# Kernel tuning notes

Hardware: AMD Instinct MI355X
Metric: run time of the kernel (lower is better)

## Reference

```python
import jax, jax.numpy as jnp
import numpy as np

K_WRITE = 4
NUM_SLOTS = 16
VOCAB = 50257
D = 512


def layer_norm(x, g, b, eps=1e-5):
    mu = jnp.mean(x, axis=-1, keepdims=True)
    var = jnp.mean((x - mu) ** 2, axis=-1, keepdims=True)
    return (x - mu) * jax.lax.rsqrt(var + eps) * g + b


def setup_inputs() -> dict:
    key = jax.random.key(0)
    ks = jax.random.split(key, 16)
    B, T = 32, 2048
    s = lambda *sh: 1.0 / np.sqrt(sh[0])
    seq = jax.random.randint(ks[0], (B, T), 0, VOCAB)
    embed = jax.random.normal(ks[1], (VOCAB, D), jnp.float32) * 0.02
    W1 = jax.random.normal(ks[2], (D, 2 * D), jnp.float32) * s(D)
    b1 = jnp.zeros((2 * D,), jnp.float32)
    W2 = jax.random.normal(ks[3], (2 * D, D), jnp.float32) * s(2 * D)
    b2 = jnp.zeros((D,), jnp.float32)
    ln_g = jnp.ones((D,), jnp.float32)
    ln_b = jnp.zeros((D,), jnp.float32)
    Wg = jax.random.normal(ks[4], (D, NUM_SLOTS), jnp.float32) * s(D)
    bg = jnp.zeros((NUM_SLOTS,), jnp.float32)
    Wr = jax.random.normal(ks[5], (D, D), jnp.float32) * s(D)
    br = jnp.zeros((D,), jnp.float32)
    Wo = jax.random.normal(ks[6], (D, VOCAB), jnp.float32) * s(D)
    bo = jnp.zeros((VOCAB,), jnp.float32)
    return dict(seq=seq, embed=embed, W1=W1, b1=b1, W2=W2, b2=b2, ln_g=ln_g,
                ln_b=ln_b, Wg=Wg, bg=bg, Wr=Wr, br=br, Wo=Wo, bo=bo)


def forward(seq, embed, W1, b1, W2, b2, ln_g, ln_b, Wg, bg, Wr, br, Wo, bo):
    # Encoder: embed -> FFN residual -> layernorm
    h = embed[seq]                                  # [B,T,D]
    ff = jax.nn.relu(h @ W1 + b1) @ W2 + b2
    hiddens = layer_norm(h + ff, ln_g, ln_b)        # [B,T,D]

    ctx_h = hiddens[:, :-1, :]                      # [B,T-1,D]
    B, Tm1, Dd = ctx_h.shape
    k_w = min(K_WRITE, Tm1)

    # write_to_memory: gate -> topk -> gather -> scatter into zero memory
    gate_scores = jnp.mean(ctx_h @ Wg + bg, axis=-1)          # [B,T-1]
    _, top_idx = jax.lax.top_k(gate_scores, k_w)              # [B,k_w]
    gathered = jnp.take_along_axis(ctx_h, top_idx[:, :, None], axis=1)  # [B,k_w,D]
    slot_idx = jnp.arange(k_w) % NUM_SLOTS                    # unique since k_w<=slots
    mem = jnp.zeros((B, NUM_SLOTS, Dd), ctx_h.dtype).at[:, slot_idx, :].set(gathered)

    # small attention read
    q = hiddens[:, -1, :] @ Wr + br                 # [B,D]
    scores = jnp.einsum('bsd,bd->bs', mem, q)       # [B,slots]
    attn = jax.nn.softmax(scores, axis=-1)
    ctx = jnp.einsum('bs,bsd->bd', attn, mem)       # [B,D]
    return ctx @ Wo + bo                            # [B,vocab]


def reference(seq, embed, W1, b1, W2, b2, ln_g, ln_b, Wg, bg, Wr, br, Wo, bo):
    return forward(seq, embed, W1, b1, W2, b2, ln_g, ln_b, Wg, bg, Wr, br, Wo, bo)
```

## Files before the change

### kernel.cpp

```cpp
#include <hip/hip_runtime.h>
#include <stdint.h>

typedef __attribute__((ext_vector_type(8))) short bf16x8;
typedef __attribute__((ext_vector_type(4))) float f32x4;
typedef __attribute__((ext_vector_type(16))) float f32x16;
typedef unsigned short ushortT;

#define DEV static __device__ __forceinline__

DEV unsigned short f2bf(float x) {
  union { float f; unsigned u; } v; v.f = x;
  unsigned r = v.u + 0x7fffu + ((v.u >> 16) & 1u);
  return (unsigned short)(r >> 16);
}
DEV float bf2f(unsigned short b) {
  union { unsigned u; float f; } v; v.u = ((unsigned)b) << 16; return v.f;
}
DEV void gll16(const void* g, void* l) {
  __builtin_amdgcn_global_load_lds((const __attribute__((address_space(1))) void*)g,
                                   (__attribute__((address_space(3))) void*)l, 16, 0, 0);
}

#define VMW(n) asm volatile("s_waitcnt vmcnt(" #n ")" ::: "memory")
#define RAWBAR() __builtin_amdgcn_s_barrier()
#define SCHED0() __builtin_amdgcn_sched_barrier(0)

__global__ void kPrep(const float* __restrict__ W1, const float* __restrict__ W2,
                      const float* __restrict__ Wg, const float* __restrict__ ln_g,
                      ushortT* __restrict__ W1t, ushortT* __restrict__ W2t,
                      float* __restrict__ gw, float* __restrict__ wgm) {
  const size_t t = (size_t)blockIdx.x * 256 + threadIdx.x;
  if (t < 524288) {
    int n = (int)(t & 1023), k = (int)(t >> 10);
    W1t[(size_t)n * 512 + k] = f2bf(W1[(size_t)k * 1024 + n]);
  } else if (t < 1048576) {
    size_t u = t - 524288;
    int n = (int)(u & 511), k = (int)(u >> 9);
    W2t[(size_t)n * 1024 + k] = f2bf(W2[(size_t)k * 512 + n]);
  } else if (t < 1048576 + 512) {
    int c = (int)(t - 1048576);
    float s = 0.f;
    for (int j = 0; j < 16; ++j) s += Wg[c * 16 + j];
    float m = s * (1.0f / 16.0f);
    wgm[c] = m;
    gw[c] = ln_g[c] * m;
  }
}

__global__ void kPrep2(const float* __restrict__ gw, const float* __restrict__ wgm,
                       const float* __restrict__ ln_b, const float* __restrict__ bg,
                       float* __restrict__ consts) {
  const int tid = threadIdx.x;
  float a = gw[tid];
  float c = ln_b[tid] * wgm[tid];
  #pragma unroll
  for (int s = 1; s < 64; s <<= 1) { a += __shfl_xor(a, s); c += __shfl_xor(c, s); }
  __shared__ float red[8][2];
  const int wv = tid >> 6, ln = tid & 63;
  if (ln == 0) { red[wv][0] = a; red[wv][1] = c; }
  __syncthreads();
  if (tid == 0) {
    float Cg = 0, Cb0 = 0;
    for (int k = 0; k < 8; ++k) { Cg += red[k][0]; Cb0 += red[k][1]; }
    float bgm = 0;
    for (int j = 0; j < 16; ++j) bgm += bg[j];
    bgm *= (1.0f / 16.0f);
    consts[0] = Cg; consts[1] = Cb0 + bgm; consts[2] = bgm;
  }
}

__global__ void kEmbed(const int* __restrict__ seq, const float* __restrict__ embed,
                       ushortT* __restrict__ h) {
  const size_t t = (size_t)blockIdx.x * 256 + threadIdx.x;
  const size_t row = t >> 6;
  const int seg = (int)(t & 63) * 8;
  const int tok = seq[row];
  const float4* src = (const float4*)(embed + (size_t)tok * 512 + seg);
  float4 x = src[0], y = src[1];
  uint4 u;
  u.x = (unsigned)f2bf(x.x) | ((unsigned)f2bf(x.y) << 16);
  u.y = (unsigned)f2bf(x.z) | ((unsigned)f2bf(x.w) << 16);
  u.z = (unsigned)f2bf(y.x) | ((unsigned)f2bf(y.y) << 16);
  u.w = (unsigned)f2bf(y.z) | ((unsigned)f2bf(y.w) << 16);
  *(uint4*)(h + row * 512 + seg) = u;
}

__global__ __launch_bounds__(512, 2) void kG1p(const ushortT* __restrict__ h,
                                               const ushortT* __restrict__ W1t,
                                               const float* __restrict__ b1,
                                               ushortT* __restrict__ Y) {
  __shared__ __align__(16) ushortT SH[32768];
  const int tid = threadIdx.x, w = tid >> 6, l = tid & 63;
  const int b = blockIdx.x, xcd = b & 7, loc = b >> 3;
  const int nt = loc & 3, mtl = loc >> 2;
  const size_t m0 = (size_t)(xcd * 16 + mtl) * 256;
  const int n0 = nt * 256;
  const int rl = l & 15, gq = l >> 4;
  f32x4 acc[4][8] = {};

  auto stage = [&](int buf, int k0) {
    #pragma unroll
    for (int q = 0; q < 2; ++q) {
      const int c = w * 2 + q;
      gll16(h + (m0 + c * 16 + rl) * 512 + k0 + gq * 8, &SH[buf * 8192 + c * 512]);
      gll16(W1t + (size_t)(n0 + c * 16 + rl) * 512 + k0 + gq * 8, &SH[16384 + buf * 8192 + c * 512]);
    }
  };

  const int wr = w >> 1, wc = w & 1, l8 = l * 8;
  auto compute = [&](int buf) {
    bf16x8 a[4], bb[8];
    #pragma unroll
    for (int i = 0; i < 4; ++i)
      a[i] = *(const bf16x8*)&SH[buf * 8192 + (wr * 4 + i) * 512 + l8];
    #pragma unroll
    for (int j = 0; j < 8; ++j)
      bb[j] = *(const bf16x8*)&SH[16384 + buf * 8192 + (wc * 8 + j) * 512 + l8];
    #pragma unroll
    for (int i = 0; i < 4; ++i)
      #pragma unroll
      for (int j = 0; j < 8; ++j)
        acc[i][j] = __builtin_amdgcn_mfma_f32_16x16x32_bf16(a[i], bb[j], acc[i][j], 0, 0, 0);
  };

  stage(0, 0); stage(1, 32);
  for (int t = 0; t < 14; ++t) {
    VMW(4); RAWBAR(); SCHED0();
    compute(t & 1);
    SCHED0(); RAWBAR();
    stage(t & 1, (t + 2) * 32);
  }
  VMW(4); RAWBAR(); SCHED0(); compute(0); SCHED0(); RAWBAR();
  VMW(0); RAWBAR(); SCHED0(); compute(1);

  float bv[8];
  #pragma unroll
  for (int j = 0; j < 8; ++j) bv[j] = b1[n0 + wc * 128 + j * 16 + rl];

  #pragma unroll
  for (int P = 0; P < 4; ++P) {
    __syncthreads();
    if (wr == P) {
      #pragma unroll
      for (int i = 0; i < 4; ++i) {
        #pragma unroll
        for (int j = 0; j < 8; ++j) {
          const int cl = wc * 128 + j * 16 + rl;
          #pragma unroll
          for (int r = 0; r < 4; ++r) {
            const int lr = i * 16 + gq * 4 + r;
            float v = acc[i][j][r] + bv[j];
            v = v > 0.0f ? v : 0.0f;
            SH[lr * 266 + cl] = f2bf(v);
          }
        }
      }
    }
    __syncthreads();
    #pragma unroll
    for (int it = 0; it < 4; ++it) {
      const int row = it * 16 + (tid >> 5);
      const int c8 = (tid & 31) * 8;
      uint4 v = *(const uint4*)&SH[row * 266 + c8];
      *(uint4*)&Y[(m0 + P * 64 + row) * 1024 + n0 + c8] = v;
    }
  }
}

__global__ __launch_bounds__(512, 2) void kG2p(const ushortT* __restrict__ Yb,
                                               const ushortT* __restrict__ W2t,
                                               const ushortT* __restrict__ h,
                                               const float* __restrict__ b2,
                                               const float* __restrict__ gw,
                                               float* __restrict__ partS, int R0) {
  __shared__ __align__(16) ushortT As[2][256 * 32];
  __shared__ __align__(16) ushortT Bs[2][256 * 32];
  __shared__ float part[256][2][3];
  const int tid = threadIdx.x, w = tid >> 6, l = tid & 63;
  const int b = blockIdx.x, xcd = b & 7, loc = b >> 3;
  const int nt = loc & 1, mtl = loc >> 1;
  const size_t m0 = (size_t)(xcd * 16 + mtl) * 256;
  const int n0 = nt * 256;
  const int rl = l & 15, gq = l >> 4;
  f32x4 acc[4][8] = {};

  auto stage = [&](int buf, int k0) {
    #pragma unroll
    for (int q = 0; q < 2; ++q) {
      const int c = w * 2 + q;
      gll16(Yb + (m0 + c * 16 + rl) * 1024 + k0 + gq * 8, &As[buf][c * 512]);
      gll16(W2t + (size_t)(n0 + c * 16 + rl) * 1024 + k0 + gq * 8, &Bs[buf][c * 512]);
    }
  };

  const int wr = w >> 1, wc = w & 1, l8 = l * 8;
  auto compute = [&](int buf) {
    bf16x8 a[4], bb[8];
    #pragma unroll
    for (int i = 0; i < 4; ++i)
      a[i] = *(const bf16x8*)&As[buf][(wr * 4 + i) * 512 + l8];
    #pragma unroll
    for (int j = 0; j < 8; ++j)
      bb[j] = *(const bf16x8*)&Bs[buf][(wc * 8 + j) * 512 + l8];
    #pragma unroll
    for (int i = 0; i < 4; ++i)
      #pragma unroll
      for (int j = 0; j < 8; ++j)
        acc[i][j] = __builtin_amdgcn_mfma_f32_16x16x32_bf16(a[i], bb[j], acc[i][j], 0, 0, 0);
  };

  stage(0, 0); stage(1, 32);
  for (int t = 0; t < 30; ++t) {
    VMW(4); RAWBAR(); SCHED0();
    compute(t & 1);
    SCHED0(); RAWBAR();
    stage(t & 1, (t + 2) * 32);
  }
  VMW(4); RAWBAR(); SCHED0(); compute(0); SCHED0(); RAWBAR();
  VMW(0); RAWBAR(); SCHED0(); compute(1);

  #pragma unroll
  for (int i = 0; i < 4; ++i) {
    #pragma unroll
    for (int r = 0; r < 4; ++r) {
      const int rowl = wr * 64 + i * 16 + gq * 4 + r;
      const size_t grow = (size_t)R0 + m0 + rowl;
      float s1 = 0, s2 = 0, s3 = 0;
      #pragma unroll
      for (int j = 0; j < 8; ++j) {
        const int col = n0 + wc * 128 + j * 16 + rl;
        const float z = acc[i][j][r] + b2[col] + bf2f(h[grow * 512 + col]);
        s1 += z; s2 += z * z; s3 += z * gw[col];
      }
      #pragma unroll
      for (int s = 1; s < 16; s <<= 1) {
        s1 += __shfl_xor(s1, s);
        s2 += __shfl_xor(s2, s);
        s3 += __shfl_xor(s3, s);
      }
      if (rl == 0) { part[rowl][wc][0] = s1; part[rowl][wc][1] = s2; part[rowl][wc][2] = s3; }
    }
  }
  __syncthreads();
  if (tid < 256) {
    const size_t grow = (size_t)R0 + m0 + tid;
    const float S1 = part[tid][0][0] + part[tid][1][0];
    const float S2 = part[tid][0][1] + part[tid][1][1];
    const float S3 = part[tid][0][2] + part[tid][1][2];
    float* p = partS + grow * 8 + nt * 4;
    p[0] = S1; p[1] = S2; p[2] = S3;
  }
}

__global__ void kTop(const float* __restrict__ partS, const float* __restrict__ consts,
                     float* __restrict__ scores, int* __restrict__ cidx,
                     int* __restrict__ ccnt) {
  const int b = blockIdx.x, tid = threadIdx.x;
  const float Cg = consts[0], Cb = consts[1];
  float v0 = -1e30f, v1 = -1e30f, v2 = -1e30f, v3 = -1e30f;
  for (int i = tid; i < 2047; i += 256) {
    const size_t row = (size_t)b * 2048 + i;
    const float* p = partS + row * 8;
    const float S1 = p[0] + p[4];
    const float S2 = p[1] + p[5];
    const float S3 = p[2] + p[6];
    const float mu = S1 * (1.0f / 512.0f);
    const float var = S2 * (1.0f / 512.0f) - mu * mu;
    const float x = rsqrtf(var + 1e-5f) * (S3 - mu * Cg) + Cb;
    scores[row] = x;
    if (x > v3) {
      if (x > v0)      { v3 = v2; v2 = v1; v1 = v0; v0 = x; }
      else if (x > v1) { v3 = v2; v2 = v1; v1 = x; }
      else if (x > v2) { v3 = v2; v2 = x; }
      else             { v3 = x; }
    }
  }
  __shared__ float lv[256][4];
  lv[tid][0] = v0; lv[tid][1] = v1; lv[tid][2] = v2; lv[tid][3] = v3;
  __syncthreads();
  for (int s = 128; s > 0; s >>= 1) {
    if (tid < s) {
      float m[8] = { lv[tid][0], lv[tid][1], lv[tid][2], lv[tid][3],
                     lv[tid + s][0], lv[tid + s][1], lv[tid + s][2], lv[tid + s][3] };
      #pragma unroll
      for (int k = 0; k < 4; ++k) {
        int mx = k;
        #pragma unroll
        for (int j2 = k + 1; j2 < 8; ++j2) if (m[j2] > m[mx]) mx = j2;
        const float tv = m[k]; m[k] = m[mx]; m[mx] = tv;
        lv[tid][k] = m[k];
      }
    }
    __syncthreads();
  }
  __shared__ int cnt;
  __shared__ float thr;
  if (tid == 0) { thr = lv[0][3] - 0.03f; cnt = 0; }
  __syncthreads();
  const float th = thr;
  const float* sc = scores + (size_t)b * 2048;
  for (int i = tid; i < 2047; i += 256) {
    if (sc[i] >= th) {
      const int p = atomicAdd(&cnt, 1);
      if (p < 24) cidx[b * 24 + p] = i;
    }
  }
  __syncthreads();
  if (tid == 0) ccnt[b] = cnt < 24 ? cnt : 24;
}

__global__ void kCompact(const int* __restrict__ ccnt, const int* __restrict__ cidx,
                         int* __restrict__ offs, int* __restrict__ rowsb,
                         int* __restrict__ rowsl, int* __restrict__ plast,
                         int* __restrict__ nrp) {
  const int tid = threadIdx.x;
  if (tid >= 32) return;
  int off = 0, nc = 0;
  for (int k = 0; k < 32; ++k) { const int c = ccnt[k]; if (k < tid) off += c; nc += c; }
  offs[tid] = off;
  const int cnt = ccnt[tid];
  for (int j = 0; j < cnt; ++j) { rowsb[off + j] = tid; rowsl[off + j] = cidx[tid * 24 + j]; }
  rowsb[nc + tid] = tid; rowsl[nc + tid] = 2047; plast[tid] = nc + tid;
  if (tid == 0) { offs[32] = nc; nrp[0] = nc + 32; }
}

__global__ void kGather(const int* __restrict__ nrp, const int* __restrict__ rowsb,
                        const int* __restrict__ rowsl, const int* __restrict__ seq,
                        const float* __restrict__ embed, float* __restrict__ H2) {
  const int p = blockIdx.x;
  if (p >= nrp[0]) return;
  const int b = rowsb[p], lr = rowsl[p];
  const size_t gr = (size_t)b * 2048 + lr;
  const int tok = seq[gr];
  const float* src = embed + (size_t)tok * 512;
  float* dst = H2 + (size_t)p * 512;
  for (int c = threadIdx.x; c < 512; c += 128) dst[c] = src[c];
}

__global__ __launch_bounds__(256) void kR1(const int* __restrict__ nrp,
                                           const float* __restrict__ H2,
                                           const float* __restrict__ W1,
                                           const float* __restrict__ b1,
                                           float* __restrict__ Y2) {
  const int p = blockIdx.y;
  if (p >= nrp[0]) return;
  const int col = blockIdx.x * 256 + threadIdx.x;
  __shared__ float hrow[512];
  for (int c = threadIdx.x; c < 512; c += 256) hrow[c] = H2[(size_t)p * 512 + c];
  __syncthreads();
  float a0 = 0, a1 = 0, a2 = 0, a3 = 0;
  #pragma unroll 4
  for (int k = 0; k < 512; k += 4) {
    a0 = fmaf(hrow[k + 0], W1[(size_t)(k + 0) * 1024 + col], a0);
    a1 = fmaf(hrow[k + 1], W1[(size_t)(k + 1) * 1024 + col], a1);
    a2 = fmaf(hrow[k + 2], W1[(size_t)(k + 2) * 1024 + col], a2);
    a3 = fmaf(hrow[k + 3], W1[(size_t)(k + 3) * 1024 + col], a3);
  }
  const float v = a0 + a1 + a2 + a3 + b1[col];
  Y2[(size_t)p * 1024 + col] = v > 0.0f ? v : 0.0f;
}

__global__ __launch_bounds__(256) void kR2(const int* __restrict__ nrp,
                                           const float* __restrict__ Y2,
                                           const float* __restrict__ W2,
                                           const float* __restrict__ b2,
                                           float* __restrict__ F2) {
  const int p = blockIdx.y;
  if (p >= nrp[0]) return;
  const int col = blockIdx.x * 256 + threadIdx.x;
  __shared__ float yrow[1024];
  for (int c = threadIdx.x; c < 1024; c += 256) yrow[c] = Y2[(size_t)p * 1024 + c];
  __syncthreads();
  float a0 = 0, a1 = 0, a2 = 0, a3 = 0;
  #pragma unroll 4
  for (int k = 0; k < 1024; k += 4) {
    a0 = fmaf(yrow[k + 0], W2[(size_t)(k + 0) * 512 + col], a0);
    a1 = fmaf(yrow[k + 1], W2[(size_t)(k + 1) * 512 + col], a1);
    a2 = fmaf(yrow[k + 2], W2[(size_t)(k + 2) * 512 + col], a2);
    a3 = fmaf(yrow[k + 3], W2[(size_t)(k + 3) * 512 + col], a3);
  }
  F2[(size_t)p * 512 + col] = a0 + a1 + a2 + a3 + b2[col];
}

__global__ void kR3(const int* __restrict__ nrp, const float* __restrict__ H2,
                    const float* __restrict__ F2, const float* __restrict__ ln_g,
                    const float* __restrict__ ln_b, const float* __restrict__ wgm,
                    const float* __restrict__ consts, float* __restrict__ LNR,
                    float* __restrict__ cscore) {
  const int p = blockIdx.x;
  if (p >= nrp[0]) return;
  const int tid = threadIdx.x;
  const int c0 = tid, c1 = tid + 256;
  const float z0 = H2[(size_t)p * 512 + c0] + F2[(size_t)p * 512 + c0];
  const float z1 = H2[(size_t)p * 512 + c1] + F2[(size_t)p * 512 + c1];
  float s1 = z0 + z1, s2 = z0 * z0 + z1 * z1;
  #pragma unroll
  for (int s = 1; s < 64; s <<= 1) { s1 += __shfl_xor(s1, s); s2 += __shfl_xor(s2, s); }
  __shared__ float red[4][2];
  __shared__ float stats[2];
  const int wv = tid >> 6, ln = tid & 63;
  if (ln == 0) { red[wv][0] = s1; red[wv][1] = s2; }
  __syncthreads();
  if (tid == 0) {
    const float S1 = red[0][0] + red[1][0] + red[2][0] + red[3][0];
    const float S2 = red[0][1] + red[1][1] + red[2][1] + red[3][1];
    const float mu = S1 * (1.0f / 512.0f);
    const float var = S2 * (1.0f / 512.0f) - mu * mu;
    stats[0] = mu; stats[1] = rsqrtf(var + 1e-5f);
  }
  __syncthreads();
  const float mu = stats[0], rstd = stats[1];
  const float l0 = (z0 - mu) * rstd * ln_g[c0] + ln_b[c0];
  const float l1 = (z1 - mu) * rstd * ln_g[c1] + ln_b[c1];
  LNR[(size_t)p * 512 + c0] = l0;
  LNR[(size_t)p * 512 + c1] = l1;
  float sp = l0 * wgm[c0] + l1 * wgm[c1];
  #pragma unroll
  for (int s = 1; s < 64; s <<= 1) sp += __shfl_xor(sp, s);
  if (ln == 0) red[wv][0] = sp;
  __syncthreads();
  if (tid == 0) cscore[p] = red[0][0] + red[1][0] + red[2][0] + red[3][0] + consts[2];
}

__global__ void kSel(const int* __restrict__ ccnt, const int* __restrict__ offs,
                     const int* __restrict__ rowsl, const int* __restrict__ plast,
                     const float* __restrict__ cscore, const float* __restrict__ LNR,
                     const float* __restrict__ Wr, const float* __restrict__ br,
                     float* __restrict__ ctx, ushortT* __restrict__ ctxB) {
  const int b = blockIdx.x, tid = threadIdx.x;
  __shared__ int psel[4];
  __shared__ float lnl[512];
  __shared__ float qs[512];
  __shared__ float aw[4];
  __shared__ float red[4][4];
  if (tid == 0) {
    const int cnt = ccnt[b], off = offs[b];
    float scv[24]; int lr[24]; bool tk[24];
    for (int j = 0; j < cnt; ++j) { scv[j] = cscore[off + j]; lr[j] = rowsl[off + j]; tk[j] = false; }
    for (int k = 0; k < 4; ++k) {
      int best = -1;
      for (int j = 0; j < cnt; ++j) {
        if (tk[j]) continue;
        if (best < 0 || scv[j] > scv[best] || (scv[j] == scv[best] && lr[j] < lr[best])) best = j;
      }
      tk[best] = true;
      psel[k] = off + best;
    }
  }
  __syncthreads();
  const int pl = plast[b];
  for (int c = tid; c < 512; c += 256) lnl[c] = LNR[(size_t)pl * 512 + c];
  __syncthreads();
  #pragma unroll
  for (int cc = 0; cc < 2; ++cc) {
    const int col = tid + cc * 256;
    float s = br[col];
    for (int d = 0; d < 512; ++d) s = fmaf(lnl[d], Wr[(size_t)d * 512 + col], s);
    qs[col] = s;
  }
  __syncthreads();
  const int p0 = psel[0], p1 = psel[1], p2 = psel[2], p3 = psel[3];
  float ps[4] = {0, 0, 0, 0};
  for (int d = tid; d < 512; d += 256) {
    const float qv = qs[d];
    ps[0] = fmaf(qv, LNR[(size_t)p0 * 512 + d], ps[0]);
    ps[1] = fmaf(qv, LNR[(size_t)p1 * 512 + d], ps[1]);
    ps[2] = fmaf(qv, LNR[(size_t)p2 * 512 + d], ps[2]);
    ps[3] = fmaf(qv, LNR[(size_t)p3 * 512 + d], ps[3]);
  }
  #pragma unroll
  for (int s = 1; s < 64; s <<= 1) {
    ps[0] += __shfl_xor(ps[0], s); ps[1] += __shfl_xor(ps[1], s);
    ps[2] += __shfl_xor(ps[2], s); ps[3] += __shfl_xor(ps[3], s);
  }
  const int wv = tid >> 6, ln = tid & 63;
  if (ln == 0) { red[wv][0] = ps[0]; red[wv][1] = ps[1]; red[wv][2] = ps[2]; red[wv][3] = ps[3]; }
  __syncthreads();
  if (tid == 0) {
    const float s0 = red[0][0] + red[1][0] + red[2][0] + red[3][0];
    const float s1 = red[0][1] + red[1][1] + red[2][1] + red[3][1];
    const float s2 = red[0][2] + red[1][2] + red[2][2] + red[3][2];
    const float s3 = red[0][3] + red[1][3] + red[2][3] + red[3][3];
    const float m = fmaxf(fmaxf(fmaxf(s0, s1), fmaxf(s2, s3)), 0.0f);
    const float e0 = expf(s0 - m), e1 = expf(s1 - m), e2 = expf(s2 - m), e3 = expf(s3 - m);
    const float den = e0 + e1 + e2 + e3 + 12.0f * expf(-m);
    aw[0] = e0 / den; aw[1] = e1 / den; aw[2] = e2 / den; aw[3] = e3 / den;
  }
  __syncthreads();
  const float a0 = aw[0], a1 = aw[1], a2 = aw[2], a3 = aw[3];
  #pragma unroll
  for (int cc = 0; cc < 2; ++cc) {
    const int col = tid + cc * 256;
    const float v = a0 * LNR[(size_t)p0 * 512 + col] + a1 * LNR[(size_t)p1 * 512 + col]
                  + a2 * LNR[(size_t)p2 * 512 + col] + a3 * LNR[(size_t)p3 * 512 + col];
    ctx[(size_t)b * 512 + col] = v;
    ctxB[(size_t)b * 512 + col] = f2bf(v);
  }
}

__global__ __launch_bounds__(512) void kOutM(const ushortT* __restrict__ ctxB,
                                             const float* __restrict__ Wo,
                                             float* __restrict__ partial) {
  const int tid = threadIdx.x, w = tid >> 6, l = tid & 63;
  const int ky = blockIdx.y;
  int col = blockIdx.x * 256 + w * 32 + (l & 31);
  const bool cv = col < 50257;
  if (!cv) col = 50256;
  const int kg = (l >> 5) * 8;
  const int kb = ky * 128;
  bf16x8 afr[8];
  #pragma unroll
  for (int ks = 0; ks < 8; ++ks)
    afr[ks] = *(const bf16x8*)&ctxB[(size_t)(l & 31) * 512 + kb + ks * 16 + kg];
  f32x16 acc = {};
  #pragma unroll
  for (int ks = 0; ks < 8; ++ks) {
    const float* wp = Wo + (size_t)(kb + ks * 16 + kg) * 50257 + col;
    float wv[8];
    #pragma unroll
    for (int j = 0; j < 8; ++j) wv[j] = wp[(size_t)j * 50257];
    bf16x8 bfr;
    #pragma unroll
    for (int j = 0; j < 8; ++j) bfr[j] = (short)f2bf(wv[j]);
    acc = __builtin_amdgcn_mfma_f32_32x32x16_bf16(afr[ks], bfr, acc, 0, 0, 0);
  }
  if (cv) {
    #pragma unroll
    for (int r = 0; r < 16; ++r) {
      const int row = (r & 3) + 8 * (r >> 2) + 4 * (l >> 5);
      partial[((size_t)ky * 32 + row) * 50257 + col] = acc[r];
    }
  }
}

__global__ __launch_bounds__(256) void kOutRed(const float* __restrict__ partial,
                                               const float* __restrict__ bo,
                                               float* __restrict__ out) {
  const size_t i = (size_t)blockIdx.x * 256 + threadIdx.x;
  if (i >= (size_t)32 * 50257) return;
  const int col = (int)(i % 50257);
  float s = bo[col];
  #pragma unroll
  for (int q = 0; q < 4; ++q) s += partial[(size_t)q * 32 * 50257 + i];
  out[i] = s;
}

extern "C" void kernel_launch(void* const* d_in, const int* in_sizes, int n_in,
                              void* d_out, int out_size, void* d_ws, size_t ws_size,
                              hipStream_t stream) {
  const int*   seq   = (const int*)  d_in[0];
  const float* embed = (const float*)d_in[1];
  const float* W1    = (const float*)d_in[2];
  const float* b1    = (const float*)d_in[3];
  const float* W2    = (const float*)d_in[4];
  const float* b2    = (const float*)d_in[5];
  const float* ln_g  = (const float*)d_in[6];
  const float* ln_b  = (const float*)d_in[7];
  const float* Wg    = (const float*)d_in[8];
  const float* bg    = (const float*)d_in[9];
  const float* Wr    = (const float*)d_in[10];
  const float* br    = (const float*)d_in[11];
  const float* Wo    = (const float*)d_in[12];
  const float* bo    = (const float*)d_in[13];
  float* out = (float*)d_out;
  char* ws = (char*)d_ws;

  ushortT* W1t   = (ushortT*)(ws + 0);
  ushortT* W2t   = (ushortT*)(ws + 1048576);
  float* gw      = (float*)(ws + 2097152);
  float* wgm     = (float*)(ws + 2099200);
  float* consts  = (float*)(ws + 2101248);
  ushortT* h     = (ushortT*)(ws + 2101504);
  ushortT* Ybuf  = (ushortT*)(ws + 69210368);
  float* partial = (float*)(ws + 69210368);
  float* scores  = (float*)(ws + 136319232);
  int* cidx      = (int*)(ws + 136581376);
  int* ccnt      = (int*)(ws + 136584448);
  int* offs      = (int*)(ws + 136584576);
  int* nrp       = (int*)(ws + 136584832);
  int* plast     = (int*)(ws + 136585088);
  int* rowsb     = (int*)(ws + 136585344);
  int* rowsl     = (int*)(ws + 136588672);
  float* partS   = (float*)(ws + 136592000);
  float* H2      = (float*)(ws + 136592000);
  float* Y2      = (float*)(ws + 138295936);
  float* F2      = (float*)(ws + 141703808);
  float* LNR     = (float*)(ws + 143407744);
  float* csc     = (float*)(ws + 145111680);
  float* ctxb    = (float*)(ws + 145115008);
  ushortT* ctxB  = (ushortT*)(ws + 145180544);

  kPrep <<<4098, 256, 0, stream>>>(W1, W2, Wg, ln_g, W1t, W2t, gw, wgm);
  kPrep2<<<1, 512, 0, stream>>>(gw, wgm, ln_b, bg, consts);
  kEmbed<<<16384, 256, 0, stream>>>(seq, embed, h);
  for (int c = 0; c < 2; ++c) {
    kG1p<<<512, 512, 0, stream>>>(h + (size_t)c * 32768 * 512, W1t, b1, Ybuf);
    kG2p<<<256, 512, 0, stream>>>(Ybuf, W2t, h, b2, gw, partS, c * 32768);
  }
  kTop    <<<32, 256, 0, stream>>>(partS, consts, scores, cidx, ccnt);
  kCompact<<<1, 64, 0, stream>>>(ccnt, cidx, offs, rowsb, rowsl, plast, nrp);
  kGather <<<800, 128, 0, stream>>>(nrp, rowsb, rowsl, seq, embed, H2);
  kR1<<<dim3(4, 800), 256, 0, stream>>>(nrp, H2, W1, b1, Y2);
  kR2<<<dim3(2, 800), 256, 0, stream>>>(nrp, Y2, W2, b2, F2);
  kR3<<<800, 256, 0, stream>>>(nrp, H2, F2, ln_g, ln_b, wgm, consts, LNR, csc);
  kSel<<<32, 256, 0, stream>>>(ccnt, offs, rowsl, plast, csc, LNR, Wr, br, ctxb, ctxB);
  kOutM<<<dim3(197, 4), 512, 0, stream>>>(ctxB, Wo, partial);
  kOutRed<<<(32 * 50257 + 255) / 256, 256, 0, stream>>>(partial, bo, out);
}
```

Baseline: 438.6 us.

## Tile weight transpose through LDS and fuse row gather into kR1

The weight-prep kernel now transposes W1 and W2 in 64x64 tiles staged through padded shared memory. Both the reads and the bf16 writes become coalesced, replacing the strided per-element scatter. The separate kGather launch is removed: kR1 reads the embedding row directly, and its first column block also writes H2 for later use by kR3. This saves one launch and one H2 round trip, at the cost of four blocks each reading the same embedding row.

```diff
diff --git a/kernel.cpp b/kernel.cpp
--- a/kernel.cpp
+++ b/kernel.cpp
@@ -25,25 +25,57 @@
 #define RAWBAR() __builtin_amdgcn_s_barrier()
 #define SCHED0() __builtin_amdgcn_sched_barrier(0)
 
-__global__ void kPrep(const float* __restrict__ W1, const float* __restrict__ W2,
-                      const float* __restrict__ Wg, const float* __restrict__ ln_g,
-                      ushortT* __restrict__ W1t, ushortT* __restrict__ W2t,
-                      float* __restrict__ gw, float* __restrict__ wgm) {
-  const size_t t = (size_t)blockIdx.x * 256 + threadIdx.x;
-  if (t < 524288) {
-    int n = (int)(t & 1023), k = (int)(t >> 10);
-    W1t[(size_t)n * 512 + k] = f2bf(W1[(size_t)k * 1024 + n]);
-  } else if (t < 1048576) {
-    size_t u = t - 524288;
-    int n = (int)(u & 511), k = (int)(u >> 9);
-    W2t[(size_t)n * 1024 + k] = f2bf(W2[(size_t)k * 512 + n]);
-  } else if (t < 1048576 + 512) {
-    int c = (int)(t - 1048576);
-    float s = 0.f;
-    for (int j = 0; j < 16; ++j) s += Wg[c * 16 + j];
-    float m = s * (1.0f / 16.0f);
-    wgm[c] = m;
-    gw[c] = ln_g[c] * m;
+__global__ __launch_bounds__(256) void kPrep(const float* __restrict__ W1,
+                                             const float* __restrict__ W2,
+                                             const float* __restrict__ Wg,
+                                             const float* __restrict__ ln_g,
+                                             ushortT* __restrict__ W1t,
+                                             ushortT* __restrict__ W2t,
+                                             float* __restrict__ gw,
+                                             float* __restrict__ wgm) {
+  __shared__ ushortT T[64][65];
+  const int tid = threadIdx.x, bb = blockIdx.x;
+  if (bb < 128) {
+    const int nt = bb & 15, kt = bb >> 4;
+    const int k0 = kt * 64, n0 = nt * 64;
+    #pragma unroll
+    for (int it = 0; it < 16; ++it) {
+      const int r = it * 4 + (tid >> 6);
+      const int c = tid & 63;
+      T[c][r] = f2bf(W1[(size_t)(k0 + r) * 1024 + n0 + c]);
+    }
+    __syncthreads();
+    #pragma unroll
+    for (int it = 0; it < 16; ++it) {
+      const int r = it * 4 + (tid >> 6);
+      const int c = tid & 63;
+      W1t[(size_t)(n0 + r) * 512 + k0 + c] = T[r][c];
+    }
+  } else if (bb < 256) {
+    const int u = bb - 128;
+    const int nt = u & 7, kt = u >> 3;
+    const int k0 = kt * 64, n0 = nt * 64;
+    #pragma unroll
+    for (int it = 0; it < 16; ++it) {
+      const int r = it * 4 + (tid >> 6);
+      const int c = tid & 63;
+      T[c][r] = f2bf(W2[(size_t)(k0 + r) * 512 + n0 + c]);
+    }
+    __syncthreads();
+    #pragma unroll
+    for (int it = 0; it < 16; ++it) {
+      const int r = it * 4 + (tid >> 6);
+      const int c = tid & 63;
+      W2t[(size_t)(n0 + r) * 1024 + k0 + c] = T[r][c];
+    }
+  } else {
+    for (int c = tid; c < 512; c += 256) {
+      float s = 0.f;
+      for (int j = 0; j < 16; ++j) s += Wg[c * 16 + j];
+      const float m = s * (1.0f / 16.0f);
+      wgm[c] = m;
+      gw[c] = ln_g[c] * m;
+    }
   }
 }
 
@@ -324,29 +356,27 @@
   if (tid == 0) { offs[32] = nc; nrp[0] = nc + 32; }
 }
 
-__global__ void kGather(const int* __restrict__ nrp, const int* __restrict__ rowsb,
-                        const int* __restrict__ rowsl, const int* __restrict__ seq,
-                        const float* __restrict__ embed, float* __restrict__ H2) {
-  const int p = blockIdx.x;
-  if (p >= nrp[0]) return;
-  const int b = rowsb[p], lr = rowsl[p];
-  const size_t gr = (size_t)b * 2048 + lr;
-  const int tok = seq[gr];
-  const float* src = embed + (size_t)tok * 512;
-  float* dst = H2 + (size_t)p * 512;
-  for (int c = threadIdx.x; c < 512; c += 128) dst[c] = src[c];
-}
-
 __global__ __launch_bounds__(256) void kR1(const int* __restrict__ nrp,
-                                           const float* __restrict__ H2,
+                                           const int* __restrict__ rowsb,
+                                           const int* __restrict__ rowsl,
+                                           const int* __restrict__ seq,
+                                           const float* __restrict__ embed,
+                                           float* __restrict__ H2,
                                            const float* __restrict__ W1,
                                            const float* __restrict__ b1,
                                            float* __restrict__ Y2) {
   const int p = blockIdx.y;
   if (p >= nrp[0]) return;
+  const int b = rowsb[p], lr = rowsl[p];
+  const int tok = seq[(size_t)b * 2048 + lr];
+  const float* src = embed + (size_t)tok * 512;
   const int col = blockIdx.x * 256 + threadIdx.x;
   __shared__ float hrow[512];
-  for (int c = threadIdx.x; c < 512; c += 256) hrow[c] = H2[(size_t)p * 512 + c];
+  for (int c = threadIdx.x; c < 512; c += 256) {
+    const float v = src[c];
+    hrow[c] = v;
+    if (blockIdx.x == 0) H2[(size_t)p * 512 + c] = v;
+  }
   __syncthreads();
   float a0 = 0, a1 = 0, a2 = 0, a3 = 0;
   #pragma unroll 4
@@ -590,7 +620,7 @@
   float* ctxb    = (float*)(ws + 145115008);
   ushortT* ctxB  = (ushortT*)(ws + 145180544);
 
-  kPrep <<<4098, 256, 0, stream>>>(W1, W2, Wg, ln_g, W1t, W2t, gw, wgm);
+  kPrep <<<257, 256, 0, stream>>>(W1, W2, Wg, ln_g, W1t, W2t, gw, wgm);
   kPrep2<<<1, 512, 0, stream>>>(gw, wgm, ln_b, bg, consts);
   kEmbed<<<16384, 256, 0, stream>>>(seq, embed, h);
   for (int c = 0; c < 2; ++c) {
@@ -599,8 +629,7 @@
   }
   kTop    <<<32, 256, 0, stream>>>(partS, consts, scores, cidx, ccnt);
   kCompact<<<1, 64, 0, stream>>>(ccnt, cidx, offs, rowsb, rowsl, plast, nrp);
-  kGather <<<800, 128, 0, stream>>>(nrp, rowsb, rowsl, seq, embed, H2);
-  kR1<<<dim3(4, 800), 256, 0, stream>>>(nrp, H2, W1, b1, Y2);
+  kR1<<<dim3(4, 800), 256, 0, stream>>>(nrp, rowsb, rowsl, seq, embed, H2, W1, b1, Y2);
   kR2<<<dim3(2, 800), 256, 0, stream>>>(nrp, Y2, W2, b2, F2);
   kR3<<<800, 256, 0, stream>>>(nrp, H2, F2, ln_g, ln_b, wgm, consts, LNR, csc);
   kSel<<<32, 256, 0, stream>>>(ccnt, offs, rowsl, plast, csc, LNR, Wr, br, ctxb, ctxB);
```

Measured after the change: 434.2 us. Within noise of the previous version (-1.0%).
